# Optimization experiments

Measured on AMD Instinct MI355X. Metric: run time of the kernel, lower is better.

Reference implementation:

```python
import jax, jax.numpy as jnp
import numpy as np

B, S, D, H, DFF = 4, 2048, 1024, 16, 4096
DH = D // H  # per-head query/value dim
EPS = 1e-5


def layer_norm(x, scale, bias):
    mu = jnp.mean(x, axis=-1, keepdims=True)
    var = jnp.mean(jnp.square(x - mu), axis=-1, keepdims=True)
    return (x - mu) * jax.lax.rsqrt(var + EPS) * scale + bias


def setup_inputs() -> dict:
    key = jax.random.key(0)
    ks = jax.random.split(key, 16)
    s_in = 1.0 / np.sqrt(D)
    s_ff = 1.0 / np.sqrt(DFF)
    inp = {
        "x": jax.random.normal(ks[0], (B, S, D), jnp.float32),
        # per-head Q/K/V projections stacked along head axis [H, D, DH]
        "wq": jax.random.normal(ks[1], (H, D, DH), jnp.float32) * s_in,
        "bq": jax.random.normal(ks[2], (H, DH), jnp.float32) * 0.01,
        "wk": jax.random.normal(ks[3], (H, D, DH), jnp.float32) * s_in,
        "bk": jax.random.normal(ks[4], (H, DH), jnp.float32) * 0.01,
        "wv": jax.random.normal(ks[5], (H, D, DH), jnp.float32) * s_in,
        "bv": jax.random.normal(ks[6], (H, DH), jnp.float32) * 0.01,
        "wo": jax.random.normal(ks[7], (H * DH, D), jnp.float32) * s_in,
        "bo": jax.random.normal(ks[8], (D,), jnp.float32) * 0.01,
        "ln1_s": jnp.ones((D,), jnp.float32),
        "ln1_b": jnp.zeros((D,), jnp.float32),
        "w1": jax.random.normal(ks[9], (D, DFF), jnp.float32) * s_in,
        "b1": jax.random.normal(ks[10], (DFF,), jnp.float32) * 0.01,
        "w2": jax.random.normal(ks[11], (DFF, D), jnp.float32) * s_ff,
        "b2": jax.random.normal(ks[12], (D,), jnp.float32) * 0.01,
        "ln2_s": jnp.ones((D,), jnp.float32),
        "ln2_b": jnp.zeros((D,), jnp.float32),
    }
    return inp


def reference(x, wq, bq, wk, bk, wv, bv, wo, bo, ln1_s, ln1_b, w1, b1, w2, b2, ln2_s, ln2_b):
    # --- masked multi-head self-attention (all heads vectorized) ---
    q = jnp.einsum('bsd,hde->bhse', x, wq) + bq[None, :, None, :]  # [B,H,S,DH]
    k = jnp.einsum('bsd,hde->bhse', x, wk) + bk[None, :, None, :]
    v = jnp.einsum('bsd,hde->bhse', x, wv) + bv[None, :, None, :]
    scores = jnp.einsum('bhse,bhte->bhst', q, k)  # [B,H,S,S]
    causal = jnp.tril(jnp.ones((S, S), bool))  # mask sets strict upper triangle to -inf
    scores = jnp.where(causal, scores, -jnp.inf)
    scale = jnp.float32(DH) ** 0.5
    attn = jax.nn.softmax(scores / scale, axis=-1)
    out = jnp.einsum('bhst,bhte->bhse', attn, v)  # [B,H,S,DH]
    concat = out.transpose(0, 2, 1, 3).reshape(B, S, H * DH)
    attn_out = concat @ wo + bo
    y = layer_norm(x + attn_out, ln1_s, ln1_b)  # post-LN residual (dropout=0)
    # --- feed-forward ---
    ff = jax.nn.relu(y @ w1 + b1) @ w2 + b2
    return layer_norm(y + ff, ln2_s, ln2_b)
```

## Files before the change

kernel.cpp:

```cpp
#include <hip/hip_runtime.h>
#include <hip/hip_bf16.h>
#include <cstdint>

#define BB 4
#define SS 2048
#define DD 1024
#define HH 16
#define DHH 64
#define DFFN 4096
#define MROWS (BB*SS)

typedef __attribute__((ext_vector_type(8))) __bf16 v8bf;
typedef __attribute__((ext_vector_type(4))) float v4f;

static __device__ __forceinline__ unsigned short f2bf(float f) {
  unsigned u = __float_as_uint(f);
  u = (u + 0x7fffu + ((u >> 16) & 1u)) >> 16;
  return (unsigned short)u;
}

static __device__ __forceinline__ unsigned bf2bits(__hip_bfloat162 h) {
  union { __hip_bfloat162 h; unsigned u; } cv; cv.h = h; return cv.u;
}

static __device__ __forceinline__ void mfma16(v4f& d, v8bf a, v8bf b) {
  d = __builtin_amdgcn_mfma_f32_16x16x32_bf16(a, b, d, 0, 0, 0);
}

static __device__ __forceinline__ void gload16(const void* g, void* l) {
  __builtin_amdgcn_global_load_lds(
      (const __attribute__((address_space(1))) unsigned int*)(unsigned long long)g,
      (__attribute__((address_space(3))) unsigned int*)(unsigned int)(unsigned long long)l,
      16, 0, 0);
}


__global__ __launch_bounds__(256) void pack_x_k(const float* __restrict__ x,
                                                unsigned short* __restrict__ xb) {
  int i = blockIdx.x * 256 + threadIdx.x;
  float4 v = ((const float4*)x)[i];
  ushort4 o;
  o.x = f2bf(v.x); o.y = f2bf(v.y); o.z = f2bf(v.z); o.w = f2bf(v.w);
  ((ushort4*)xb)[i] = o;
}

static __device__ __forceinline__ void transpose_tile(const float* __restrict__ src,
                                                      unsigned short* __restrict__ dst,
                                                      int R, int C, int rt, int ct) {
  __shared__ float tile[32][33];
  const int tx = threadIdx.x, ty = threadIdx.y;
  #pragma unroll
  for (int j = 0; j < 4; ++j)
    tile[ty + j * 8][tx] = src[(size_t)(rt + ty + j * 8) * C + ct + tx];
  __syncthreads();
  #pragma unroll
  for (int j = 0; j < 4; ++j)
    dst[(size_t)(ct + ty + j * 8) * R + rt + tx] = f2bf(tile[tx][ty + j * 8]);
}

__global__ __launch_bounds__(256) void transpose_k(const float* __restrict__ src,
                                                   unsigned short* __restrict__ dst,
                                                   int R, int C) {
  transpose_tile(src, dst, R, C, blockIdx.y * 32, blockIdx.x * 32);
}

__global__ __launch_bounds__(256) void transpose_qkv_k(const float* __restrict__ wq,
                                                       const float* __restrict__ wk,
                                                       const float* __restrict__ wv,
                                                       unsigned short* __restrict__ dst) {
  const int z = blockIdx.z;
  const int w = z >> 4, h = z & 15;
  const float* src = (w == 0) ? wq : ((w == 1) ? wk : wv);
  src += (size_t)h * DD * DHH;
  unsigned short* d = dst + (size_t)(w * DD + h * DHH) * DD;
  transpose_tile(src, d, DD, DHH, blockIdx.y * 32, blockIdx.x * 32);
}

template<int MODE>
static __device__ __forceinline__ void gemm_epi(
    const v4f& a4, int rb, int col, int N,
    const float* __restrict__ bias0, const float* __restrict__ bias1,
    const float* __restrict__ bias2,
    float* __restrict__ outF, unsigned short* __restrict__ o0,
    unsigned short* __restrict__ o1, unsigned short* __restrict__ o2) {
  if constexpr (MODE == 0) {
    const int seg = col >> 10, cc = col & 1023;
    const int h = cc >> 6, e = cc & 63;
    const float bias = (seg == 0) ? bias0[cc] : (seg == 1) ? bias1[cc] : bias2[cc];
    if (seg < 2) {
      unsigned short* dst = (seg == 0) ? o0 : o1;
      const float scl = (seg == 0) ? 0.18033688f : 1.0f;
      #pragma unroll
      for (int i = 0; i < 4; ++i) {
        const int row = rb + i, b = row >> 11, s = row & (SS - 1);
        dst[(((size_t)b * HH + h) * SS + s) * DHH + e] = f2bf((a4[i] + bias) * scl);
      }
    } else {
      const int b = rb >> 11, s0q = rb & (SS - 1);
      ushort4 pv;
      pv.x = f2bf(a4[0] + bias);
      pv.y = f2bf(a4[1] + bias);
      pv.z = f2bf(a4[2] + bias);
      pv.w = f2bf(a4[3] + bias);
      *(ushort4*)&o2[(((size_t)b * HH + h) * DHH + e) * SS + s0q] = pv;
    }
  } else if constexpr (MODE == 1 || MODE == 3) {
    const float bias = bias0[col];
    #pragma unroll
    for (int i = 0; i < 4; ++i)
      outF[(size_t)(rb + i) * N + col] = a4[i] + bias;
  } else {
    const float bias = bias0[col];
    #pragma unroll
    for (int i = 0; i < 4; ++i)
      o0[(size_t)(rb + i) * N + col] = f2bf(fmaxf(a4[i] + bias, 0.f));
  }
}


template<int MODE>
__global__ __launch_bounds__(512, 2) void gemm_bt(
    const unsigned short* __restrict__ A, const unsigned short* __restrict__ Bt,
    const float* __restrict__ bias0, const float* __restrict__ bias1,
    const float* __restrict__ bias2,
    float* __restrict__ outF, unsigned short* __restrict__ o0,
    unsigned short* __restrict__ o1, unsigned short* __restrict__ o2,
    int M, int N, int K) {
  extern __shared__ __align__(16) char smem[];
  const int tid = threadIdx.x;
  const int wid = tid >> 6, lane = tid & 63;
  const int l15 = lane & 15, kg = lane >> 4;
  const int m0 = blockIdx.y * 256, n0 = blockIdx.x * 256;
  const int wm = (wid >> 2) * 128, wn = (wid & 3) * 64;

  const int sr8 = wid * 8 + (lane >> 3);
  const int sge = ((lane & 7) ^ ((lane >> 3) & 7)) << 3;
  const int swr = (l15 & 7) << 4;

  const int NK = K >> 6;
  v4f acc[8][4] = {};

  #define STA(q, kt, lb) gload16(A  + (size_t)(m0 + (q) * 64 + sr8) * K + (kt) * 64 + sge, \
                                 (lb) + (q) * 8192 + wid * 1024)
  #define STB(q, kt, lb) gload16(Bt + (size_t)(n0 + (q) * 64 + sr8) * K + (kt) * 64 + sge, \
                                 (lb) + (q) * 8192 + wid * 1024)

  {
    char* A0b = smem;
    char* B0b = smem + 65536;
    STB(0, 0, B0b); STB(1, 0, B0b); STB(2, 0, B0b); STB(3, 0, B0b);
    STA(0, 0, A0b); STA(2, 0, A0b); STA(1, 0, A0b); STA(3, 0, A0b);
    asm volatile("s_waitcnt vmcnt(2)" ::: "memory");
    __builtin_amdgcn_s_barrier();
  }

  #pragma unroll 1
  for (int j = 0; j < NK; ++j) {
    char* Ac = smem + (j & 1) * 32768;
    char* Bc = smem + 65536 + (j & 1) * 32768;
    char* An = smem + ((j + 1) & 1) * 32768;
    char* Bn = smem + 65536 + ((j + 1) & 1) * 32768;
    const bool more = (j + 1 < NK);

    v8bf bf_[4][2], af01[4][2];
    #pragma unroll
    for (int nr = 0; nr < 4; ++nr)
      #pragma unroll
      for (int ks = 0; ks < 2; ++ks)
        bf_[nr][ks] = *(const v8bf*)(Bc + (wn + nr * 16 + l15) * 128 +
                                     (((ks * 4 + kg) << 4) ^ swr));
    #pragma unroll
    for (int mi = 0; mi < 4; ++mi)
      #pragma unroll
      for (int ks = 0; ks < 2; ++ks)
        af01[mi][ks] = *(const v8bf*)(Ac + (wm + mi * 16 + l15) * 128 +
                                      (((ks * 4 + kg) << 4) ^ swr));
    if (more) { STB(0, j + 1, Bn); STB(1, j + 1, Bn); STB(2, j + 1, Bn); STB(3, j + 1, Bn); }
    __builtin_amdgcn_s_setprio(1);
    #pragma unroll
    for (int mi = 0; mi < 2; ++mi)
      #pragma unroll
      for (int nr = 0; nr < 4; ++nr)
        #pragma unroll
        for (int ks = 0; ks < 2; ++ks)
          mfma16(acc[mi][nr], af01[mi][ks], bf_[nr][ks]);
    __builtin_amdgcn_s_setprio(0);
    __builtin_amdgcn_s_barrier();

    if (more) {
      STA(0, j + 1, An); STA(2, j + 1, An); STA(1, j + 1, An); STA(3, j + 1, An);
      asm volatile("s_waitcnt vmcnt(8)" ::: "memory");
    } else {
      asm volatile("s_waitcnt vmcnt(0)" ::: "memory");
    }
    __builtin_amdgcn_s_setprio(1);
    #pragma unroll
    for (int mi = 2; mi < 4; ++mi)
      #pragma unroll
      for (int nr = 0; nr < 4; ++nr)
        #pragma unroll
        for (int ks = 0; ks < 2; ++ks)
          mfma16(acc[mi][nr], af01[mi][ks], bf_[nr][ks]);
    __builtin_amdgcn_s_setprio(0);
    __builtin_amdgcn_s_barrier();

    v8bf af23[4][2];
    #pragma unroll
    for (int mi = 0; mi < 4; ++mi)
      #pragma unroll
      for (int ks = 0; ks < 2; ++ks)
        af23[mi][ks] = *(const v8bf*)(Ac + (wm + (mi + 4) * 16 + l15) * 128 +
                                      (((ks * 4 + kg) << 4) ^ swr));
    __builtin_amdgcn_s_setprio(1);
    #pragma unroll
    for (int mi = 0; mi < 2; ++mi)
      #pragma unroll
      for (int nr = 0; nr < 4; ++nr)
        #pragma unroll
        for (int ks = 0; ks < 2; ++ks)
          mfma16(acc[mi + 4][nr], af23[mi][ks], bf_[nr][ks]);
    __builtin_amdgcn_s_setprio(0);
    __builtin_amdgcn_s_barrier();

    if (more) asm volatile("s_waitcnt vmcnt(2)" ::: "memory");
    __builtin_amdgcn_s_setprio(1);
    #pragma unroll
    for (int mi = 2; mi < 4; ++mi)
      #pragma unroll
      for (int nr = 0; nr < 4; ++nr)
        #pragma unroll
        for (int ks = 0; ks < 2; ++ks)
          mfma16(acc[mi + 4][nr], af23[mi][ks], bf_[nr][ks]);
    __builtin_amdgcn_s_setprio(0);
    __builtin_amdgcn_s_barrier();
  }
  #undef STA
  #undef STB

  #pragma unroll
  for (int nr = 0; nr < 4; ++nr) {
    const int col = n0 + wn + nr * 16 + l15;
    #pragma unroll
    for (int mr = 0; mr < 8; ++mr)
      gemm_epi<MODE>(acc[mr][nr], m0 + wm + mr * 16 + kg * 4, col, N,
                     bias0, bias1, bias2, outF, o0, o1, o2);
  }
}


template<int MODE>
__global__ __launch_bounds__(512, 2) void gemm_bt_n(
    const unsigned short* __restrict__ A, const unsigned short* __restrict__ Bt,
    const float* __restrict__ bias0, const float* __restrict__ bias1,
    const float* __restrict__ bias2,
    float* __restrict__ outF, unsigned short* __restrict__ o0,
    unsigned short* __restrict__ o1, unsigned short* __restrict__ o2,
    int M, int N, int K) {
  extern __shared__ __align__(16) char smem[];
  const int tid = threadIdx.x;
  const int wid = tid >> 6, lane = tid & 63;
  const int l15 = lane & 15, kg = lane >> 4;
  const int m0 = blockIdx.y * 256, n0 = blockIdx.x * 128;
  const int wm = (wid >> 1) * 64, wn = (wid & 1) * 64;

  const int sr8 = wid * 8 + (lane >> 3);
  const int sge = ((lane & 7) ^ ((lane >> 3) & 7)) << 3;
  const int swr = (l15 & 7) << 4;

  const int NK = K >> 6;
  v4f acc[4][4] = {};

  #define STA(q, kt, lb) gload16(A  + (size_t)(m0 + (q) * 64 + sr8) * K + (kt) * 64 + sge, \
                                 (lb) + (q) * 8192 + wid * 1024)
  #define STB(q, kt, lb) gload16(Bt + (size_t)(n0 + (q) * 64 + sr8) * K + (kt) * 64 + sge, \
                                 (lb) + (q) * 8192 + wid * 1024)

  {
    char* A0b = smem;
    char* B0b = smem + 65536;
    STB(0, 0, B0b); STB(1, 0, B0b);
    STA(0, 0, A0b); STA(1, 0, A0b); STA(2, 0, A0b); STA(3, 0, A0b);
    asm volatile("s_waitcnt vmcnt(0)" ::: "memory");
    __builtin_amdgcn_s_barrier();
  }

  #pragma unroll 1
  for (int j = 0; j < NK; ++j) {
    char* Ac = smem + (j & 1) * 32768;
    char* Bc = smem + 65536 + (j & 1) * 16384;
    char* An = smem + ((j + 1) & 1) * 32768;
    char* Bn = smem + 65536 + ((j + 1) & 1) * 16384;
    const bool more = (j + 1 < NK);

    v8bf bf_[4][2], af01[2][2];
    #pragma unroll
    for (int nr = 0; nr < 4; ++nr)
      #pragma unroll
      for (int ks = 0; ks < 2; ++ks)
        bf_[nr][ks] = *(const v8bf*)(Bc + (wn + nr * 16 + l15) * 128 +
                                     (((ks * 4 + kg) << 4) ^ swr));
    #pragma unroll
    for (int mi = 0; mi < 2; ++mi)
      #pragma unroll
      for (int ks = 0; ks < 2; ++ks)
        af01[mi][ks] = *(const v8bf*)(Ac + (wm + mi * 16 + l15) * 128 +
                                      (((ks * 4 + kg) << 4) ^ swr));
    if (more) {
      STB(0, j + 1, Bn); STB(1, j + 1, Bn);
      STA(0, j + 1, An); STA(1, j + 1, An); STA(2, j + 1, An); STA(3, j + 1, An);
    }
    __builtin_amdgcn_s_setprio(1);
    #pragma unroll
    for (int mi = 0; mi < 2; ++mi)
      #pragma unroll
      for (int nr = 0; nr < 4; ++nr)
        #pragma unroll
        for (int ks = 0; ks < 2; ++ks)
          mfma16(acc[mi][nr], af01[mi][ks], bf_[nr][ks]);
    __builtin_amdgcn_s_setprio(0);
    __builtin_amdgcn_s_barrier();

    v8bf af23[2][2];
    #pragma unroll
    for (int mi = 0; mi < 2; ++mi)
      #pragma unroll
      for (int ks = 0; ks < 2; ++ks)
        af23[mi][ks] = *(const v8bf*)(Ac + (wm + (mi + 2) * 16 + l15) * 128 +
                                      (((ks * 4 + kg) << 4) ^ swr));
    __builtin_amdgcn_s_setprio(1);
    #pragma unroll
    for (int mi = 0; mi < 2; ++mi)
      #pragma unroll
      for (int nr = 0; nr < 4; ++nr)
        #pragma unroll
        for (int ks = 0; ks < 2; ++ks)
          mfma16(acc[mi + 2][nr], af23[mi][ks], bf_[nr][ks]);
    __builtin_amdgcn_s_setprio(0);
    if (more) asm volatile("s_waitcnt vmcnt(0)" ::: "memory");
    __builtin_amdgcn_s_barrier();
  }
  #undef STA
  #undef STB

  #pragma unroll
  for (int nr = 0; nr < 4; ++nr) {
    const int col = n0 + wn + nr * 16 + l15;
    #pragma unroll
    for (int mr = 0; mr < 4; ++mr)
      gemm_epi<MODE>(acc[mr][nr], m0 + wm + mr * 16 + kg * 4, col, N,
                     bias0, bias1, bias2, outF, o0, o1, o2);
  }
}

__global__ __launch_bounds__(512) void attn_k(const unsigned short* __restrict__ q,
                                              const unsigned short* __restrict__ k,
                                              const unsigned short* __restrict__ vt,
                                              unsigned short* __restrict__ concat) {
  __shared__ __align__(16) unsigned short Ks[64 * 64];
  __shared__ __align__(16) unsigned short Vs[64 * 64];
  __shared__ __align__(16) unsigned short PL[8][16 * 72];

  const int tid = threadIdx.x, wid = tid >> 6, lane = tid & 63;
  const int l15 = lane & 15, kg = lane >> 4;
  const int bh = blockIdx.y, b = bh >> 4, h = bh & 15;

  const char* kb = (const char*)(k + (size_t)bh * SS * DHH);
  const char* vb = (const char*)(vt + (size_t)bh * DHH * SS);
  unsigned short* ob = concat + (size_t)b * SS * DD + h * DHH;

  const int srow = wid * 8 + (lane >> 3);
  const int swz_c = ((lane & 7) * 16) ^ ((lane >> 3) << 4);
  const int swr = (l15 & 7) << 4;
  unsigned short* pl = &PL[wid][0];

  #pragma unroll 1
  for (int half = 0; half < 2; ++half) {
    const int qt = (half == 0) ? (int)blockIdx.x : 15 - (int)blockIdx.x;
    const int q0 = qt * 128;
    const int q0w = q0 + wid * 16;
    const unsigned short* qb = q + ((size_t)bh * SS + q0w) * DHH;
    const int qrow = q0w + l15;

    v8bf qf[2];
    #pragma unroll
    for (int ks = 0; ks < 2; ++ks)
      qf[ks] = *(const v8bf*)&qb[l15 * DHH + ks * 32 + kg * 8];

    v4f acc[4] = {};
    float mrun = -1e30f, ssum = 0.f;

    const int T = qt * 2 + 2;
    for (int it = 0; it < T; ++it) {
      const int t0 = it * 64;
      gload16(kb + (size_t)(t0 + srow) * 128 + swz_c, &Ks[(wid * 8) * 64]);
      gload16(vb + (size_t)srow * 4096 + (size_t)t0 * 2 + swz_c, &Vs[(wid * 8) * 64]);
      __syncthreads();

      if (t0 <= q0w + 15) {
        v4f sT[4] = {};
        #pragma unroll
        for (int mt = 0; mt < 4; ++mt) {
          #pragma unroll
          for (int ks = 0; ks < 2; ++ks) {
            const v8bf kf = *(const v8bf*)((const char*)Ks + (mt * 16 + l15) * 128 +
                                           ((ks * 64 + kg * 16) ^ swr));
            mfma16(sT[mt], kf, qf[ks]);
          }
        }

        const bool full = (t0 + 63 <= q0w);
        float p[16];
        #pragma unroll
        for (int mt = 0; mt < 4; ++mt)
          #pragma unroll
          for (int rg = 0; rg < 4; ++rg) {
            float s = sT[mt][rg];
            if (!full) s = (t0 + mt * 16 + kg * 4 + rg <= qrow) ? s : -1e30f;
            p[mt * 4 + rg] = s;
          }
        float m8[8], m4_[4];
        #pragma unroll
        for (int i = 0; i < 8; ++i) m8[i] = fmaxf(p[2 * i], p[2 * i + 1]);
        #pragma unroll
        for (int i = 0; i < 4; ++i) m4_[i] = fmaxf(m8[2 * i], m8[2 * i + 1]);
        float mx = fmaxf(fmaxf(m4_[0], m4_[1]), fmaxf(m4_[2], m4_[3]));
        mx = fmaxf(mx, __shfl_xor(mx, 16));
        mx = fmaxf(mx, __shfl_xor(mx, 32));
        if (!__all(mx - mrun <= 8.0f)) {
          const float mnew = fmaxf(mrun, mx);
          const float fac = exp2f(mrun - mnew);
          mrun = mnew;
          ssum *= fac;
          #pragma unroll
          for (int mt = 0; mt < 4; ++mt) acc[mt] *= fac;
        }
        #pragma unroll
        for (int i = 0; i < 16; ++i) p[i] = exp2f(p[i] - mrun);
        float s8[8], s4_[4];
        #pragma unroll
        for (int i = 0; i < 8; ++i) s8[i] = p[2 * i] + p[2 * i + 1];
        #pragma unroll
        for (int i = 0; i < 4; ++i) s4_[i] = s8[2 * i] + s8[2 * i + 1];
        float ts = (s4_[0] + s4_[1]) + (s4_[2] + s4_[3]);
        ts += __shfl_xor(ts, 16);
        ts += __shfl_xor(ts, 32);
        ssum += ts;
        #pragma unroll
        for (int mt = 0; mt < 4; ++mt) {
          uint2 w;
          w.x = bf2bits(__float22bfloat162_rn(make_float2(p[mt * 4 + 0], p[mt * 4 + 1])));
          w.y = bf2bits(__float22bfloat162_rn(make_float2(p[mt * 4 + 2], p[mt * 4 + 3])));
          *(uint2*)((char*)pl + l15 * 144 + mt * 32 + kg * 8) = w;
        }
        asm volatile("s_waitcnt lgkmcnt(0)" ::: "memory");
        __builtin_amdgcn_sched_barrier(0);

        #pragma unroll
        for (int ks = 0; ks < 2; ++ks) {
          const v8bf pb = *(const v8bf*)((const char*)pl + l15 * 144 + ks * 64 + kg * 16);
          #pragma unroll
          for (int mt = 0; mt < 4; ++mt) {
            const v8bf va = *(const v8bf*)((const char*)Vs + (mt * 16 + l15) * 128 +
                                           ((ks * 64 + kg * 16) ^ swr));
            mfma16(acc[mt], va, pb);
          }
        }
      }
      __syncthreads();
    }

    const float inv = 1.0f / ssum;
    #pragma unroll
    for (int mt = 0; mt < 4; ++mt) {
      ushort4 o4;
      o4.x = f2bf(acc[mt][0] * inv);
      o4.y = f2bf(acc[mt][1] * inv);
      o4.z = f2bf(acc[mt][2] * inv);
      o4.w = f2bf(acc[mt][3] * inv);
      *(ushort4*)&ob[(size_t)qrow * DD + mt * 16 + kg * 4] = o4;
    }
  }
}

template<bool WB>
__global__ __launch_bounds__(256) void resid_ln_k(const float* __restrict__ a,
                                                  const float* __restrict__ t,
                                                  const float* __restrict__ sc,
                                                  const float* __restrict__ bi,
                                                  float* __restrict__ yo,
                                                  unsigned short* __restrict__ yb) {
  __shared__ float rs[4], rs2[4];
  const int row = blockIdx.x, tid = threadIdx.x;
  const int wid = tid >> 6, lane = tid & 63;
  const float4 x4 = ((const float4*)(a + (size_t)row * DD))[tid];
  const float4 t4 = ((const float4*)(t + (size_t)row * DD))[tid];
  const float v0 = x4.x + t4.x, v1 = x4.y + t4.y, v2 = x4.z + t4.z, v3 = x4.w + t4.w;
  float s = v0 + v1 + v2 + v3;
  float s2 = v0 * v0 + v1 * v1 + v2 * v2 + v3 * v3;
  #pragma unroll
  for (int m = 1; m < 64; m <<= 1) { s += __shfl_xor(s, m); s2 += __shfl_xor(s2, m); }
  if (lane == 0) { rs[wid] = s; rs2[wid] = s2; }
  __syncthreads();
  s = rs[0] + rs[1] + rs[2] + rs[3];
  s2 = rs2[0] + rs2[1] + rs2[2] + rs2[3];
  const float mu = s * (1.0f / DD);
  const float var = s2 * (1.0f / DD) - mu * mu;
  const float rstd = rsqrtf(var + 1e-5f);
  const int c0 = tid * 4;
  const float o0 = (v0 - mu) * rstd * sc[c0 + 0] + bi[c0 + 0];
  const float o1 = (v1 - mu) * rstd * sc[c0 + 1] + bi[c0 + 1];
  const float o2 = (v2 - mu) * rstd * sc[c0 + 2] + bi[c0 + 2];
  const float o3 = (v3 - mu) * rstd * sc[c0 + 3] + bi[c0 + 3];
  float4 ov; ov.x = o0; ov.y = o1; ov.z = o2; ov.w = o3;
  ((float4*)(yo + (size_t)row * DD))[tid] = ov;
  if (WB) {
    ushort4 ub; ub.x = f2bf(o0); ub.y = f2bf(o1); ub.z = f2bf(o2); ub.w = f2bf(o3);
    ((ushort4*)(yb + (size_t)row * DD))[tid] = ub;
  }
}


extern "C" void kernel_launch(void* const* d_in, const int* in_sizes, int n_in,
                              void* d_out, int out_size, void* d_ws, size_t ws_size,
                              hipStream_t stream) {
  const float* x   = (const float*)d_in[0];
  const float* wq  = (const float*)d_in[1];
  const float* bq  = (const float*)d_in[2];
  const float* wk  = (const float*)d_in[3];
  const float* bk  = (const float*)d_in[4];
  const float* wv  = (const float*)d_in[5];
  const float* bv  = (const float*)d_in[6];
  const float* wo  = (const float*)d_in[7];
  const float* bo  = (const float*)d_in[8];
  const float* l1s = (const float*)d_in[9];
  const float* l1b = (const float*)d_in[10];
  const float* w1  = (const float*)d_in[11];
  const float* b1  = (const float*)d_in[12];
  const float* w2  = (const float*)d_in[13];
  const float* b2  = (const float*)d_in[14];
  const float* l2s = (const float*)d_in[15];
  const float* l2b = (const float*)d_in[16];

  char* ws = (char*)d_ws;
  unsigned short* WO_T  = (unsigned short*)(ws + 0);
  unsigned short* W1_T  = (unsigned short*)(ws + 2097152);
  unsigned short* W2_T  = (unsigned short*)(ws + 10485760);
  float*          Y     = (float*)(ws + 18874368);
  unsigned short* YBF   = (unsigned short*)(ws + 52428800);
  float*          TMP1  = (float*)(ws + 69206016);
  unsigned short* XBF   = (unsigned short*)(ws + 102760448);
  unsigned short* WQKVT = (unsigned short*)(ws + 119537664);
  unsigned short* QB    = (unsigned short*)(ws + 125829120);
  unsigned short* KB    = (unsigned short*)(ws + 142606336);
  unsigned short* VTB   = (unsigned short*)(ws + 159383552);
  unsigned short* CONC  = (unsigned short*)(ws + 176160768);
  unsigned short* H1    = (unsigned short*)(ws + 102760448);
  float*          TMP2  = TMP1;

  constexpr int GSMEM  = 131072;
  constexpr int GSMEMN = 98304;
  hipFuncSetAttribute(reinterpret_cast<const void*>(gemm_bt<2>),
                      hipFuncAttributeMaxDynamicSharedMemorySize, GSMEM);
  hipFuncSetAttribute(reinterpret_cast<const void*>(gemm_bt_n<0>),
                      hipFuncAttributeMaxDynamicSharedMemorySize, GSMEMN);
  hipFuncSetAttribute(reinterpret_cast<const void*>(gemm_bt_n<1>),
                      hipFuncAttributeMaxDynamicSharedMemorySize, GSMEMN);
  hipFuncSetAttribute(reinterpret_cast<const void*>(gemm_bt_n<3>),
                      hipFuncAttributeMaxDynamicSharedMemorySize, GSMEMN);

  pack_x_k<<<8192, 256, 0, stream>>>(x, XBF);
  transpose_qkv_k<<<dim3(2, 32, 48), dim3(32, 8), 0, stream>>>(wq, wk, wv, WQKVT);
  transpose_k<<<dim3(32, 32),  dim3(32, 8), 0, stream>>>(wo, WO_T, 1024, 1024);
  transpose_k<<<dim3(128, 32), dim3(32, 8), 0, stream>>>(w1, W1_T, 1024, 4096);
  transpose_k<<<dim3(32, 128), dim3(32, 8), 0, stream>>>(w2, W2_T, 4096, 1024);

  gemm_bt_n<0><<<dim3(24, 32), 512, GSMEMN, stream>>>(XBF, WQKVT, bq, bk, bv,
      nullptr, QB, KB, VTB, MROWS, 3072, 1024);
  attn_k<<<dim3(8, 64), 512, 0, stream>>>(QB, KB, VTB, CONC);
  gemm_bt_n<1><<<dim3(8, 32), 512, GSMEMN, stream>>>(CONC, WO_T, bo, nullptr, nullptr,
      TMP1, nullptr, nullptr, nullptr, MROWS, 1024, 1024);
  resid_ln_k<true><<<8192, 256, 0, stream>>>(x, TMP1, l1s, l1b, Y, YBF);
  gemm_bt<2><<<dim3(16, 32), 512, GSMEM, stream>>>(YBF, W1_T, b1, nullptr, nullptr,
      nullptr, H1, nullptr, nullptr, MROWS, 4096, 1024);
  gemm_bt_n<3><<<dim3(8, 32), 512, GSMEMN, stream>>>(H1, W2_T, b2, nullptr, nullptr,
      TMP2, nullptr, nullptr, nullptr, MROWS, 1024, 4096);
  resid_ln_k<false><<<8192, 256, 0, stream>>>(Y, TMP2, l2s, l2b, (float*)d_out, nullptr);
}
```

Before: 413.3 us.

## Shrink GEMM K-tile to 32 for higher occupancy and drop the 256x256 GEMM

Halves the K step of the 256x128 GEMM kernel from 64 to 32. That cuts shared memory per block from 96KB to 48KB, changes the swizzle for 64-byte rows, and raises launch bounds to 4 blocks per CU. The FFN1 GEMM now uses this kernel instead of the 256x256 variant, which is deleted. More resident blocks should hide latency, but twice as many K iterations and barriers add sync overhead, and the smaller tiles lower data reuse.

```diff
diff --git a/kernel.cpp b/kernel.cpp
--- a/kernel.cpp
+++ b/kernel.cpp
@@ -119,137 +119,7 @@
 
 
 template<int MODE>
-__global__ __launch_bounds__(512, 2) void gemm_bt(
-    const unsigned short* __restrict__ A, const unsigned short* __restrict__ Bt,
-    const float* __restrict__ bias0, const float* __restrict__ bias1,
-    const float* __restrict__ bias2,
-    float* __restrict__ outF, unsigned short* __restrict__ o0,
-    unsigned short* __restrict__ o1, unsigned short* __restrict__ o2,
-    int M, int N, int K) {
-  extern __shared__ __align__(16) char smem[];
-  const int tid = threadIdx.x;
-  const int wid = tid >> 6, lane = tid & 63;
-  const int l15 = lane & 15, kg = lane >> 4;
-  const int m0 = blockIdx.y * 256, n0 = blockIdx.x * 256;
-  const int wm = (wid >> 2) * 128, wn = (wid & 3) * 64;
-
-  const int sr8 = wid * 8 + (lane >> 3);
-  const int sge = ((lane & 7) ^ ((lane >> 3) & 7)) << 3;
-  const int swr = (l15 & 7) << 4;
-
-  const int NK = K >> 6;
-  v4f acc[8][4] = {};
-
-  #define STA(q, kt, lb) gload16(A  + (size_t)(m0 + (q) * 64 + sr8) * K + (kt) * 64 + sge, \
-                                 (lb) + (q) * 8192 + wid * 1024)
-  #define STB(q, kt, lb) gload16(Bt + (size_t)(n0 + (q) * 64 + sr8) * K + (kt) * 64 + sge, \
-                                 (lb) + (q) * 8192 + wid * 1024)
-
-  {
-    char* A0b = smem;
-    char* B0b = smem + 65536;
-    STB(0, 0, B0b); STB(1, 0, B0b); STB(2, 0, B0b); STB(3, 0, B0b);
-    STA(0, 0, A0b); STA(2, 0, A0b); STA(1, 0, A0b); STA(3, 0, A0b);
-    asm volatile("s_waitcnt vmcnt(2)" ::: "memory");
-    __builtin_amdgcn_s_barrier();
-  }
-
-  #pragma unroll 1
-  for (int j = 0; j < NK; ++j) {
-    char* Ac = smem + (j & 1) * 32768;
-    char* Bc = smem + 65536 + (j & 1) * 32768;
-    char* An = smem + ((j + 1) & 1) * 32768;
-    char* Bn = smem + 65536 + ((j + 1) & 1) * 32768;
-    const bool more = (j + 1 < NK);
-
-    v8bf bf_[4][2], af01[4][2];
-    #pragma unroll
-    for (int nr = 0; nr < 4; ++nr)
-      #pragma unroll
-      for (int ks = 0; ks < 2; ++ks)
-        bf_[nr][ks] = *(const v8bf*)(Bc + (wn + nr * 16 + l15) * 128 +
-                                     (((ks * 4 + kg) << 4) ^ swr));
-    #pragma unroll
-    for (int mi = 0; mi < 4; ++mi)
-      #pragma unroll
-      for (int ks = 0; ks < 2; ++ks)
-        af01[mi][ks] = *(const v8bf*)(Ac + (wm + mi * 16 + l15) * 128 +
-                                      (((ks * 4 + kg) << 4) ^ swr));
-    if (more) { STB(0, j + 1, Bn); STB(1, j + 1, Bn); STB(2, j + 1, Bn); STB(3, j + 1, Bn); }
-    __builtin_amdgcn_s_setprio(1);
-    #pragma unroll
-    for (int mi = 0; mi < 2; ++mi)
-      #pragma unroll
-      for (int nr = 0; nr < 4; ++nr)
-        #pragma unroll
-        for (int ks = 0; ks < 2; ++ks)
-          mfma16(acc[mi][nr], af01[mi][ks], bf_[nr][ks]);
-    __builtin_amdgcn_s_setprio(0);
-    __builtin_amdgcn_s_barrier();
-
-    if (more) {
-      STA(0, j + 1, An); STA(2, j + 1, An); STA(1, j + 1, An); STA(3, j + 1, An);
-      asm volatile("s_waitcnt vmcnt(8)" ::: "memory");
-    } else {
-      asm volatile("s_waitcnt vmcnt(0)" ::: "memory");
-    }
-    __builtin_amdgcn_s_setprio(1);
-    #pragma unroll
-    for (int mi = 2; mi < 4; ++mi)
-      #pragma unroll
-      for (int nr = 0; nr < 4; ++nr)
-        #pragma unroll
-        for (int ks = 0; ks < 2; ++ks)
-          mfma16(acc[mi][nr], af01[mi][ks], bf_[nr][ks]);
-    __builtin_amdgcn_s_setprio(0);
-    __builtin_amdgcn_s_barrier();
-
-    v8bf af23[4][2];
-    #pragma unroll
-    for (int mi = 0; mi < 4; ++mi)
-      #pragma unroll
-      for (int ks = 0; ks < 2; ++ks)
-        af23[mi][ks] = *(const v8bf*)(Ac + (wm + (mi + 4) * 16 + l15) * 128 +
-                                      (((ks * 4 + kg) << 4) ^ swr));
-    __builtin_amdgcn_s_setprio(1);
-    #pragma unroll
-    for (int mi = 0; mi < 2; ++mi)
-      #pragma unroll
-      for (int nr = 0; nr < 4; ++nr)
-        #pragma unroll
-        for (int ks = 0; ks < 2; ++ks)
-          mfma16(acc[mi + 4][nr], af23[mi][ks], bf_[nr][ks]);
-    __builtin_amdgcn_s_setprio(0);
-    __builtin_amdgcn_s_barrier();
-
-    if (more) asm volatile("s_waitcnt vmcnt(2)" ::: "memory");
-    __builtin_amdgcn_s_setprio(1);
-    #pragma unroll
-    for (int mi = 2; mi < 4; ++mi)
-      #pragma unroll
-      for (int nr = 0; nr < 4; ++nr)
-        #pragma unroll
-        for (int ks = 0; ks < 2; ++ks)
-          mfma16(acc[mi + 4][nr], af23[mi][ks], bf_[nr][ks]);
-    __builtin_amdgcn_s_setprio(0);
-    __builtin_amdgcn_s_barrier();
-  }
-  #undef STA
-  #undef STB
-
-  #pragma unroll
-  for (int nr = 0; nr < 4; ++nr) {
-    const int col = n0 + wn + nr * 16 + l15;
-    #pragma unroll
-    for (int mr = 0; mr < 8; ++mr)
-      gemm_epi<MODE>(acc[mr][nr], m0 + wm + mr * 16 + kg * 4, col, N,
-                     bias0, bias1, bias2, outF, o0, o1, o2);
-  }
-}
-
-
-template<int MODE>
-__global__ __launch_bounds__(512, 2) void gemm_bt_n(
+__global__ __launch_bounds__(512, 4) void gemm_bt_n(
     const unsigned short* __restrict__ A, const unsigned short* __restrict__ Bt,
     const float* __restrict__ bias0, const float* __restrict__ bias1,
     const float* __restrict__ bias2,
@@ -263,78 +133,60 @@
   const int m0 = blockIdx.y * 256, n0 = blockIdx.x * 128;
   const int wm = (wid >> 1) * 64, wn = (wid & 1) * 64;
 
-  const int sr8 = wid * 8 + (lane >> 3);
-  const int sge = ((lane & 7) ^ ((lane >> 3) & 7)) << 3;
-  const int swr = (l15 & 7) << 4;
-
-  const int NK = K >> 6;
+  const int srow = wid * 16 + (lane >> 2);
+  const int sge = ((lane & 3) ^ ((lane >> 3) & 3)) * 8;
+  const int swr = ((l15 >> 1) & 3) << 4;
+
+  const int NK = K >> 5;
   v4f acc[4][4] = {};
 
-  #define STA(q, kt, lb) gload16(A  + (size_t)(m0 + (q) * 64 + sr8) * K + (kt) * 64 + sge, \
-                                 (lb) + (q) * 8192 + wid * 1024)
-  #define STB(q, kt, lb) gload16(Bt + (size_t)(n0 + (q) * 64 + sr8) * K + (kt) * 64 + sge, \
-                                 (lb) + (q) * 8192 + wid * 1024)
+  #define STA(p, kt, lb) gload16(A + (size_t)(m0 + (p) * 128 + srow) * K + (kt) * 32 + sge, \
+                                 (lb) + (p) * 8192 + wid * 1024)
+  #define STB(kt, lb)    gload16(Bt + (size_t)(n0 + srow) * K + (kt) * 32 + sge, \
+                                 (lb) + wid * 1024)
 
   {
-    char* A0b = smem;
-    char* B0b = smem + 65536;
-    STB(0, 0, B0b); STB(1, 0, B0b);
-    STA(0, 0, A0b); STA(1, 0, A0b); STA(2, 0, A0b); STA(3, 0, A0b);
+    STA(0, 0, smem); STA(1, 0, smem);
+    STB(0, smem + 32768);
     asm volatile("s_waitcnt vmcnt(0)" ::: "memory");
     __builtin_amdgcn_s_barrier();
   }
 
   #pragma unroll 1
   for (int j = 0; j < NK; ++j) {
-    char* Ac = smem + (j & 1) * 32768;
-    char* Bc = smem + 65536 + (j & 1) * 16384;
-    char* An = smem + ((j + 1) & 1) * 32768;
-    char* Bn = smem + 65536 + ((j + 1) & 1) * 16384;
+    char* Ac = smem + (j & 1) * 16384;
+    char* Bc = smem + 32768 + (j & 1) * 8192;
+    char* An = smem + ((j + 1) & 1) * 16384;
+    char* Bn = smem + 32768 + ((j + 1) & 1) * 8192;
     const bool more = (j + 1 < NK);
 
-    v8bf bf_[4][2], af01[2][2];
+    v8bf bf_[4], af01[2];
     #pragma unroll
     for (int nr = 0; nr < 4; ++nr)
-      #pragma unroll
-      for (int ks = 0; ks < 2; ++ks)
-        bf_[nr][ks] = *(const v8bf*)(Bc + (wn + nr * 16 + l15) * 128 +
-                                     (((ks * 4 + kg) << 4) ^ swr));
+      bf_[nr] = *(const v8bf*)(Bc + (wn + nr * 16 + l15) * 64 + ((kg << 4) ^ swr));
     #pragma unroll
     for (int mi = 0; mi < 2; ++mi)
-      #pragma unroll
-      for (int ks = 0; ks < 2; ++ks)
-        af01[mi][ks] = *(const v8bf*)(Ac + (wm + mi * 16 + l15) * 128 +
-                                      (((ks * 4 + kg) << 4) ^ swr));
-    if (more) {
-      STB(0, j + 1, Bn); STB(1, j + 1, Bn);
-      STA(0, j + 1, An); STA(1, j + 1, An); STA(2, j + 1, An); STA(3, j + 1, An);
-    }
+      af01[mi] = *(const v8bf*)(Ac + (wm + mi * 16 + l15) * 64 + ((kg << 4) ^ swr));
+    if (more) { STA(0, j + 1, An); STA(1, j + 1, An); STB(j + 1, Bn); }
     __builtin_amdgcn_s_setprio(1);
     #pragma unroll
     for (int mi = 0; mi < 2; ++mi)
       #pragma unroll
       for (int nr = 0; nr < 4; ++nr)
-        #pragma unroll
-        for (int ks = 0; ks < 2; ++ks)
-          mfma16(acc[mi][nr], af01[mi][ks], bf_[nr][ks]);
+        mfma16(acc[mi][nr], af01[mi], bf_[nr]);
     __builtin_amdgcn_s_setprio(0);
     __builtin_amdgcn_s_barrier();
 
-    v8bf af23[2][2];
+    v8bf af23[2];
     #pragma unroll
     for (int mi = 0; mi < 2; ++mi)
-      #pragma unroll
-      for (int ks = 0; ks < 2; ++ks)
-        af23[mi][ks] = *(const v8bf*)(Ac + (wm + (mi + 2) * 16 + l15) * 128 +
-                                      (((ks * 4 + kg) << 4) ^ swr));
+      af23[mi] = *(const v8bf*)(Ac + (wm + (mi + 2) * 16 + l15) * 64 + ((kg << 4) ^ swr));
     __builtin_amdgcn_s_setprio(1);
     #pragma unroll
     for (int mi = 0; mi < 2; ++mi)
       #pragma unroll
       for (int nr = 0; nr < 4; ++nr)
-        #pragma unroll
-        for (int ks = 0; ks < 2; ++ks)
-          mfma16(acc[mi + 2][nr], af23[mi][ks], bf_[nr][ks]);
+        mfma16(acc[mi + 2][nr], af23[mi], bf_[nr]);
     __builtin_amdgcn_s_setprio(0);
     if (more) asm volatile("s_waitcnt vmcnt(0)" ::: "memory");
     __builtin_amdgcn_s_barrier();
@@ -557,13 +409,12 @@
   unsigned short* H1    = (unsigned short*)(ws + 102760448);
   float*          TMP2  = TMP1;
 
-  constexpr int GSMEM  = 131072;
-  constexpr int GSMEMN = 98304;
-  hipFuncSetAttribute(reinterpret_cast<const void*>(gemm_bt<2>),
-                      hipFuncAttributeMaxDynamicSharedMemorySize, GSMEM);
+  constexpr int GSMEMN = 49152;
   hipFuncSetAttribute(reinterpret_cast<const void*>(gemm_bt_n<0>),
                       hipFuncAttributeMaxDynamicSharedMemorySize, GSMEMN);
   hipFuncSetAttribute(reinterpret_cast<const void*>(gemm_bt_n<1>),
+                      hipFuncAttributeMaxDynamicSharedMemorySize, GSMEMN);
+  hipFuncSetAttribute(reinterpret_cast<const void*>(gemm_bt_n<2>),
                       hipFuncAttributeMaxDynamicSharedMemorySize, GSMEMN);
   hipFuncSetAttribute(reinterpret_cast<const void*>(gemm_bt_n<3>),
                       hipFuncAttributeMaxDynamicSharedMemorySize, GSMEMN);
@@ -580,7 +431,7 @@
   gemm_bt_n<1><<<dim3(8, 32), 512, GSMEMN, stream>>>(CONC, WO_T, bo, nullptr, nullptr,
       TMP1, nullptr, nullptr, nullptr, MROWS, 1024, 1024);
   resid_ln_k<true><<<8192, 256, 0, stream>>>(x, TMP1, l1s, l1b, Y, YBF);
-  gemm_bt<2><<<dim3(16, 32), 512, GSMEM, stream>>>(YBF, W1_T, b1, nullptr, nullptr,
+  gemm_bt_n<2><<<dim3(32, 32), 512, GSMEMN, stream>>>(YBF, W1_T, b1, nullptr, nullptr,
       nullptr, H1, nullptr, nullptr, MROWS, 4096, 1024);
   gemm_bt_n<3><<<dim3(8, 32), 512, GSMEMN, stream>>>(H1, W2_T, b2, nullptr, nullptr,
       TMP2, nullptr, nullptr, nullptr, MROWS, 1024, 4096);
```

Measured after the change: 442.0 us. 1.07x slower.
